# Kernel optimization log

Measured on AMD Instinct MI355X. Metric: run time of the kernel, lower is better.

The kernel has to match this reference:

```python
import jax, jax.numpy as jnp
import numpy as np

N = 100000   # num nodes
E = 3200000  # num edges (avg degree 32)
EPS = 1e-5   # BatchNorm eps


def _gcn_norm(edge_index, edge_weight, n):
    # add self loops with weight 1 (PyG gcn_norm default fill_value=1.0)
    loops = jnp.arange(n, dtype=edge_index.dtype)
    ei = jnp.concatenate([edge_index, jnp.stack([loops, loops])], axis=1)
    ew = jnp.concatenate([edge_weight, jnp.ones((n,), edge_weight.dtype)])
    row, col = ei[0], ei[1]
    deg = jax.ops.segment_sum(ew, col, num_segments=n)
    deg_safe = jnp.where(deg > 0, deg, 1.0)
    dinv = jnp.where(deg > 0, jax.lax.rsqrt(deg_safe), 0.0)
    norm = dinv[row] * ew * dinv[col]  # [E+N]
    return row, col, norm


def _gcn_conv(x, row, col, norm, W, b, n):
    h = x @ W                                   # [N, out]
    msg = h[row] * norm[:, None]                # gather + scale, [E+N, out]
    out = jax.ops.segment_sum(msg, col, num_segments=n)  # scatter-add
    return out + b


def _bn(x, g, b, rm, rv):
    # BatchNorm1d in eval mode: running statistics
    return (x - rm) * jax.lax.rsqrt(rv + EPS) * g + b


def setup_inputs() -> dict:
    key = jax.random.key(0)
    ks = jax.random.split(key, 24)
    def p(i, shape, scale=1.0):
        return jax.random.normal(ks[i], shape, dtype=jnp.float32) * scale
    inp = {
        "x": p(0, (N, 1)),
        "edge_index": jax.random.randint(ks[1], (2, E), 0, N, dtype=jnp.int32),
        "edge_weight": jax.random.uniform(ks[2], (E,), dtype=jnp.float32),
        # GCNConv weights (glorot-ish scale) and biases
        "W1": p(3, (1, 16), 0.5), "b1": jnp.zeros((16,), jnp.float32),
        "W2": p(4, (16, 4), 0.25), "b2": jnp.zeros((4,), jnp.float32),
        "W3": p(5, (4, 1), 0.5), "b3": jnp.zeros((1,), jnp.float32),
        # BatchNorm params + running stats (running_var > 0)
        "g1": p(6, (16,), 0.1) + 1.0, "be1": p(7, (16,), 0.1),
        "rm1": p(8, (16,), 0.1), "rv1": jax.random.uniform(ks[9], (16,)) + 0.5,
        "g2": p(10, (4,), 0.1) + 1.0, "be2": p(11, (4,), 0.1),
        "rm2": p(12, (4,), 0.1), "rv2": jax.random.uniform(ks[13], (4,)) + 0.5,
        "g3": p(14, (1,), 0.1) + 1.0, "be3": p(15, (1,), 0.1),
        "rm3": p(16, (1,), 0.1), "rv3": jax.random.uniform(ks[17], (1,)) + 0.5,
        # end Linear(1, 1)
        "Wl": p(18, (1, 1)), "bl": p(19, (1,), 0.1),
    }
    return inp


def reference(x, edge_index, edge_weight,
              W1, b1, W2, b2, W3, b3,
              g1, be1, rm1, rv1,
              g2, be2, rm2, rv2,
              g3, be3, rm3, rv3,
              Wl, bl):
    row, col, norm = _gcn_norm(edge_index, edge_weight, N)
    h = _gcn_conv(x, row, col, norm, W1, b1, N)
    h = jax.nn.relu(_bn(h, g1, be1, rm1, rv1))  # dropout = identity in eval
    h = _gcn_conv(h, row, col, norm, W2, b2, N)
    h = jax.nn.relu(_bn(h, g2, be2, rm2, rv2))
    h = _gcn_conv(h, row, col, norm, W3, b3, N)
    h = _bn(h, g3, be3, rm3, rv3)
    h = h @ Wl + bl
    return jax.nn.sigmoid(h)
```

## Files before the change

### kernel.cpp

```cpp
#include <hip/hip_runtime.h>
#include <math.h>

#define NN 100000
#define NE 3200000
#define EPSBN 1e-5f

#define BSH 7
#define NB 782
#define NBLK 500
#define CHUNK 6400
#define C4 (CHUNK/4)
#define CAP 5120
#define BTA 512

#define NSB 12512
#define STCAP 4608

__global__ void k_params_zero(const float* __restrict__ W1, const float* __restrict__ b1,
                              const float* __restrict__ g1, const float* __restrict__ be1,
                              const float* __restrict__ rm1, const float* __restrict__ rv1,
                              const float* __restrict__ b2,
                              const float* __restrict__ g2, const float* __restrict__ be2,
                              const float* __restrict__ rm2, const float* __restrict__ rv2,
                              const float* __restrict__ b3,
                              const float* __restrict__ g3, const float* __restrict__ be3,
                              const float* __restrict__ rm3, const float* __restrict__ rv3,
                              const float* __restrict__ Wl, const float* __restrict__ bl,
                              float* __restrict__ P, int* __restrict__ cnt) {
    int f = threadIdx.x;
    for (int i = f; i < NB; i += 1024) cnt[i] = 0;
    if (f < 16) {
        float k = g1[f] * rsqrtf(rv1[f] + EPSBN);
        P[f]      = W1[f] * k;
        P[16 + f] = (b1[f] - rm1[f]) * k + be1[f];
    }
    if (f < 4) {
        float k = g2[f] * rsqrtf(rv2[f] + EPSBN);
        P[32 + f] = k;
        P[36 + f] = (b2[f] - rm2[f]) * k + be2[f];
    }
    if (f == 0) {
        float k = g3[0] * rsqrtf(rv3[0] + EPSBN);
        P[40] = k * Wl[0];
        P[41] = ((b3[0] - rm3[0]) * k + be3[0]) * Wl[0] + bl[0];
    }
}

__global__ void k_build(const int* __restrict__ row, const int* __restrict__ col,
                        const float* __restrict__ ew, int* __restrict__ cnt,
                        uint2* __restrict__ rec) {
    __shared__ int h[NB];
    __shared__ int gb[NB];
    __shared__ int gsum[98];
    __shared__ uint2 st[CHUNK];
    __shared__ unsigned short sb[CHUNK];
    int blk = blockIdx.x, tid = threadIdx.x;
    for (int j = tid; j < NB; j += BTA) h[j] = 0;
    __syncthreads();

    const int4* c4 = (const int4*)(col + blk * CHUNK);
    int rk[4][4];
#pragma unroll
    for (int it = 0; it < 4; ++it) {
        int i = tid + it * BTA;
        if (i < C4) {
            int4 c = c4[i];
            rk[it][0] = atomicAdd(&h[c.x >> BSH], 1);
            rk[it][1] = atomicAdd(&h[c.y >> BSH], 1);
            rk[it][2] = atomicAdd(&h[c.z >> BSH], 1);
            rk[it][3] = atomicAdd(&h[c.w >> BSH], 1);
        }
    }
    __syncthreads();

    for (int j = tid; j < NB; j += BTA) {
        int hj = h[j];
        gb[j] = hj ? atomicAdd(&cnt[j], hj) : 0;
    }

    if (tid < 98) {
        int s = 0, b0 = tid * 8;
#pragma unroll
        for (int k = 0; k < 8; ++k) { int idx = b0 + k; s += (idx < NB) ? h[idx] : 0; }
        gsum[tid] = s;
    }
    __syncthreads();
    if (tid == 0) {
        int run = 0;
        for (int g = 0; g < 98; ++g) { int t = gsum[g]; gsum[g] = run; run += t; }
    }
    __syncthreads();
    if (tid < 98) {
        int run = gsum[tid], b0 = tid * 8;
#pragma unroll
        for (int k = 0; k < 8; ++k) {
            int idx = b0 + k;
            if (idx < NB) { int t = h[idx]; h[idx] = run; run += t; }
        }
    }
    __syncthreads();

    const int4*   r4 = (const int4*)(row + blk * CHUNK);
    const float4* w4 = (const float4*)(ew + blk * CHUNK);
#pragma unroll
    for (int it = 0; it < 4; ++it) {
        int i = tid + it * BTA;
        if (i < C4) {
            int4 c = c4[i]; int4 r = r4[i]; float4 w = w4[i];
            int b0 = c.x >> BSH, b1 = c.y >> BSH, b2 = c.z >> BSH, b3 = c.w >> BSH;
            int s0 = h[b0] + rk[it][0];
            st[s0] = make_uint2((unsigned)r.x | ((unsigned)(c.x & 127) << 17), __float_as_uint(w.x));
            sb[s0] = (unsigned short)b0;
            int s1 = h[b1] + rk[it][1];
            st[s1] = make_uint2((unsigned)r.y | ((unsigned)(c.y & 127) << 17), __float_as_uint(w.y));
            sb[s1] = (unsigned short)b1;
            int s2 = h[b2] + rk[it][2];
            st[s2] = make_uint2((unsigned)r.z | ((unsigned)(c.z & 127) << 17), __float_as_uint(w.z));
            sb[s2] = (unsigned short)b2;
            int s3 = h[b3] + rk[it][3];
            st[s3] = make_uint2((unsigned)r.w | ((unsigned)(c.w & 127) << 17), __float_as_uint(w.w));
            sb[s3] = (unsigned short)b3;
        }
    }
    __syncthreads();

    for (int i = tid; i < CHUNK; i += BTA) {
        int b = sb[i];
        rec[(size_t)b * CAP + gb[b] + (i - h[b])] = st[i];
    }
}

__global__ void k_subsort_deg(const int* __restrict__ cnt, uint2* __restrict__ rec,
                              int2* __restrict__ subsn, const float* __restrict__ x,
                              float* __restrict__ dinv, float* __restrict__ xd) {
    __shared__ uint2 st[STCAP];
    __shared__ int subtot[16];
    __shared__ int live[16];
    __shared__ int sstart[16];
    __shared__ int scount[16];
    int bin = blockIdx.x, tid = threadIdx.x;
    int lane = tid & 63, wv = tid >> 6;
    int n = cnt[bin];
    if (n > STCAP) n = STCAP;
    uint2* rb = rec + (size_t)bin * CAP;
    for (int i = tid; i < n; i += BTA) st[i] = rb[i];
    if (tid < 16) subtot[tid] = 0;
    __syncthreads();

    int myCnt = 0;
    for (int base = tid - lane; base < n; base += BTA) {
        int i = base + lane;
        bool v = (i < n);
        unsigned key = v ? ((st[i].x >> 20) & 15u) : 0u;
        unsigned long long bv = __ballot(v);
        unsigned long long b0 = __ballot(key & 1u);
        unsigned long long b1 = __ballot(key & 2u);
        unsigned long long b2 = __ballot(key & 4u);
        unsigned long long b3 = __ballot(key & 8u);
        if (lane < 16) {
            unsigned k = (unsigned)lane;
            unsigned long long m = bv;
            m &= (k & 1u) ? b0 : ~b0;
            m &= (k & 2u) ? b1 : ~b1;
            m &= (k & 4u) ? b2 : ~b2;
            m &= (k & 8u) ? b3 : ~b3;
            myCnt += __popcll(m);
        }
    }
    if (lane < 16 && myCnt) atomicAdd(&subtot[lane], myCnt);
    __syncthreads();

    if (tid == 0) {
        int run = 0;
        for (int k = 0; k < 16; ++k) {
            live[k] = run;
            sstart[k] = run;
            scount[k] = subtot[k];
            subsn[bin * 16 + k] = make_int2(bin * CAP + run, subtot[k]);
            run += subtot[k];
        }
    }
    __syncthreads();

    for (int base = tid - lane; base < n; base += BTA) {
        int i = base + lane;
        bool v = (i < n);
        uint2 rcd = v ? st[i] : make_uint2(0u, 0u);
        unsigned key = v ? ((rcd.x >> 20) & 15u) : 0u;
        unsigned long long bv = __ballot(v);
        unsigned long long b0 = __ballot(key & 1u);
        unsigned long long b1 = __ballot(key & 2u);
        unsigned long long b2 = __ballot(key & 4u);
        unsigned long long b3 = __ballot(key & 8u);
        int gb = 0;
        if (lane < 16) {
            unsigned k = (unsigned)lane;
            unsigned long long m = bv;
            m &= (k & 1u) ? b0 : ~b0;
            m &= (k & 2u) ? b1 : ~b1;
            m &= (k & 4u) ? b2 : ~b2;
            m &= (k & 8u) ? b3 : ~b3;
            int c = __popcll(m);
            if (c) gb = atomicAdd(&live[(int)k], c);
        }
        unsigned long long same = bv;
        same &= (key & 1u) ? b0 : ~b0;
        same &= (key & 2u) ? b1 : ~b1;
        same &= (key & 4u) ? b2 : ~b2;
        same &= (key & 8u) ? b3 : ~b3;
        unsigned long long below = (lane == 0) ? 0ull : ((~0ull) >> (64 - lane));
        int rank = __popcll(same & below);
        int mybase = __shfl(gb, (int)key);
        if (v) rb[mybase + rank] = rcd;
    }
    __syncthreads();

    for (int s = 0; s < 2; ++s) {
        int sb = (wv << 1) | s;
        int n0 = scount[sb];
        const uint2* p = rb + sstart[sb];
        float acc[8] = {0.f, 0.f, 0.f, 0.f, 0.f, 0.f, 0.f, 0.f};
        for (int i = lane; i < n0; i += 64) {
            uint2 v = p[i];
            int cl = (v.x >> 17) & 7;
            float w = __uint_as_float(v.y);
#pragma unroll
            for (int c = 0; c < 8; ++c) acc[c] += (cl == c) ? w : 0.f;
        }
#pragma unroll
        for (int c = 0; c < 8; ++c) {
            float a = acc[c];
            a += __shfl_xor(a, 1);  a += __shfl_xor(a, 2);  a += __shfl_xor(a, 4);
            a += __shfl_xor(a, 8);  a += __shfl_xor(a, 16); a += __shfl_xor(a, 32);
            acc[c] = a;
        }
        float mine = acc[0];
#pragma unroll
        for (int c = 1; c < 8; ++c) mine = (lane == c) ? acc[c] : mine;
        int colv = (bin << BSH) + (sb << 3) + lane;
        if (lane < 8 && colv < NN) {
            float d = rsqrtf(1.0f + mine);
            dinv[colv] = d;
            xd[colv] = x[colv] * d;
        }
    }
}


__global__ void k_agg1_2(const int2* __restrict__ subsn, const uint2* __restrict__ rec,
                         const float* __restrict__ dinv, const float* __restrict__ xd,
                         const float* __restrict__ P, const float* __restrict__ W2,
                         float* __restrict__ m2s) {
    __shared__ float sacc[8][8][32];
    int tid = threadIdx.x, lane = tid & 63, wv = tid >> 6;
    int b = blockIdx.x * 8 + wv;
    int2 sn = subsn[b];
    float acc[8] = {0.f, 0.f, 0.f, 0.f, 0.f, 0.f, 0.f, 0.f};
    for (int i = lane; i < sn.y; i += 64) {
        uint2 v = rec[sn.x + i];
        int cl = (v.x >> 17) & 7;
        float g = xd[v.x & 0x1FFFF] * __uint_as_float(v.y);
#pragma unroll
        for (int c = 0; c < 8; ++c) acc[c] += (cl == c) ? g : 0.f;
    }
#pragma unroll
    for (int c = 0; c < 8; ++c) acc[c] += __shfl_xor(acc[c], 32);
    if (lane < 32) {
#pragma unroll
        for (int c = 0; c < 8; ++c) sacc[wv][c][lane] = acc[c];
    }
    __syncthreads();
    if (tid < 64) {
        int w8 = tid >> 3, c = tid & 7;
        float s = 0.f;
        for (int l = 0; l < 32; ++l) s += sacc[w8][c][(l + tid) & 31];
        int colv = blockIdx.x * 64 + tid;
        if (colv < NN) {
            float dc = dinv[colv];
            float y = (s + xd[colv]) * dc;
            float m0 = 0.f, m1 = 0.f, m2v = 0.f, m3v = 0.f;
#pragma unroll
            for (int f = 0; f < 16; ++f) {
                float z = fmaxf(fmaf(y, P[f], P[16 + f]), 0.0f);
                m0 = fmaf(z, W2[f * 4 + 0], m0);
                m1 = fmaf(z, W2[f * 4 + 1], m1);
                m2v = fmaf(z, W2[f * 4 + 2], m2v);
                m3v = fmaf(z, W2[f * 4 + 3], m3v);
            }
            *(float4*)(m2s + 4 * colv) = make_float4(m0 * dc, m1 * dc, m2v * dc, m3v * dc);
        }
    }
}

__global__ void k_agg2_2(const int2* __restrict__ subsn, const uint2* __restrict__ rec,
                         const float* __restrict__ dinv, const float* __restrict__ m2s,
                         const float* __restrict__ P, const float* __restrict__ W3,
                         float* __restrict__ m3s) {
    __shared__ float sacc[8][8][4][32];
    __shared__ float sfin[8][8][4];
    int tid = threadIdx.x, lane = tid & 63, wv = tid >> 6;
    int b = blockIdx.x * 8 + wv;
    int2 sn = subsn[b];
    float acc[8][4];
#pragma unroll
    for (int c = 0; c < 8; ++c)
#pragma unroll
        for (int j = 0; j < 4; ++j) acc[c][j] = 0.f;
    for (int i = lane; i < sn.y; i += 64) {
        uint2 v = rec[sn.x + i];
        int cl = (v.x >> 17) & 7;
        float w = __uint_as_float(v.y);
        float4 m = *(const float4*)(m2s + 4 * (v.x & 0x1FFFF));
#pragma unroll
        for (int c = 0; c < 8; ++c) {
            float sel = (cl == c) ? w : 0.f;
            acc[c][0] = fmaf(m.x, sel, acc[c][0]);
            acc[c][1] = fmaf(m.y, sel, acc[c][1]);
            acc[c][2] = fmaf(m.z, sel, acc[c][2]);
            acc[c][3] = fmaf(m.w, sel, acc[c][3]);
        }
    }
#pragma unroll
    for (int c = 0; c < 8; ++c)
#pragma unroll
        for (int j = 0; j < 4; ++j) acc[c][j] += __shfl_xor(acc[c][j], 32);
    if (lane < 32) {
#pragma unroll
        for (int c = 0; c < 8; ++c)
#pragma unroll
            for (int j = 0; j < 4; ++j) sacc[wv][c][j][lane] = acc[c][j];
    }
    __syncthreads();
    if (tid < 256) {
        int w8 = tid >> 5, c = (tid >> 2) & 7, j = tid & 3;
        float s = 0.f;
        for (int l = 0; l < 32; ++l) s += sacc[w8][c][j][(l + tid) & 31];
        sfin[w8][c][j] = s;
    }
    __syncthreads();
    if (tid < 64) {
        int w8 = tid >> 3, c = tid & 7;
        int colv = blockIdx.x * 64 + tid;
        if (colv < NN) {
            float dc = dinv[colv];
            float4 mc = *(const float4*)(m2s + 4 * colv);
            float a0 = (sfin[w8][c][0] + mc.x) * dc;
            float a1 = (sfin[w8][c][1] + mc.y) * dc;
            float a2 = (sfin[w8][c][2] + mc.z) * dc;
            float a3 = (sfin[w8][c][3] + mc.w) * dc;
            float v3 = 0.f;
            v3 = fmaf(fmaxf(fmaf(a0, P[32], P[36]), 0.f), W3[0], v3);
            v3 = fmaf(fmaxf(fmaf(a1, P[33], P[37]), 0.f), W3[1], v3);
            v3 = fmaf(fmaxf(fmaf(a2, P[34], P[38]), 0.f), W3[2], v3);
            v3 = fmaf(fmaxf(fmaf(a3, P[35], P[39]), 0.f), W3[3], v3);
            m3s[colv] = v3 * dc;
        }
    }
}

__global__ void k_agg3_2(const int2* __restrict__ subsn, const uint2* __restrict__ rec,
                         const float* __restrict__ dinv, const float* __restrict__ m3s,
                         const float* __restrict__ P, float* __restrict__ out) {
    __shared__ float sacc[8][8][32];
    int tid = threadIdx.x, lane = tid & 63, wv = tid >> 6;
    int b = blockIdx.x * 8 + wv;
    int2 sn = subsn[b];
    float acc[8] = {0.f, 0.f, 0.f, 0.f, 0.f, 0.f, 0.f, 0.f};
    for (int i = lane; i < sn.y; i += 64) {
        uint2 v = rec[sn.x + i];
        int cl = (v.x >> 17) & 7;
        float g = m3s[v.x & 0x1FFFF] * __uint_as_float(v.y);
#pragma unroll
        for (int c = 0; c < 8; ++c) acc[c] += (cl == c) ? g : 0.f;
    }
#pragma unroll
    for (int c = 0; c < 8; ++c) acc[c] += __shfl_xor(acc[c], 32);
    if (lane < 32) {
#pragma unroll
        for (int c = 0; c < 8; ++c) sacc[wv][c][lane] = acc[c];
    }
    __syncthreads();
    if (tid < 64) {
        int w8 = tid >> 3, c = tid & 7;
        float s = 0.f;
        for (int l = 0; l < 32; ++l) s += sacc[w8][c][(l + tid) & 31];
        int colv = blockIdx.x * 64 + tid;
        if (colv < NN) {
            float t = fmaf((s + m3s[colv]) * dinv[colv], P[40], P[41]);
            out[colv] = 1.0f / (1.0f + __expf(-t));
        }
    }
}


__global__ void k_init_deg(float* __restrict__ deg) {
    int i = blockIdx.x * blockDim.x + threadIdx.x;
    if (i < NN) deg[i] = 1.0f;
}

__global__ void k_dinv_y1(const float* __restrict__ deg, const float* __restrict__ x,
                          float* __restrict__ dinv, float* __restrict__ y1) {
    int i = blockIdx.x * blockDim.x + threadIdx.x;
    if (i >= NN) return;
    float d = rsqrtf(deg[i]);
    dinv[i] = d;
    y1[i] = x[i] * d * d;
}

__global__ void k_l1_epi(const float* __restrict__ y1, const float* __restrict__ dinv,
                         const float* __restrict__ P, const float* __restrict__ W2,
                         float* __restrict__ m2, float* __restrict__ agg2) {
    int i = blockIdx.x * blockDim.x + threadIdx.x;
    if (i >= NN) return;
    float y = y1[i];
    float m0 = 0.f, m1 = 0.f, m2v = 0.f, m3v = 0.f;
#pragma unroll
    for (int f = 0; f < 16; ++f) {
        float z = fmaxf(fmaf(y, P[f], P[16 + f]), 0.0f);
        m0 = fmaf(z, W2[f * 4 + 0], m0);
        m1 = fmaf(z, W2[f * 4 + 1], m1);
        m2v = fmaf(z, W2[f * 4 + 2], m2v);
        m3v = fmaf(z, W2[f * 4 + 3], m3v);
    }
    float d = dinv[i];
    float d2 = d * d;
    *(float4*)(m2 + 4 * i)   = make_float4(m0, m1, m2v, m3v);
    *(float4*)(agg2 + 4 * i) = make_float4(m0 * d2, m1 * d2, m2v * d2, m3v * d2);
}

__global__ void k_l2_epi(const float* __restrict__ agg2, const float* __restrict__ dinv,
                         const float* __restrict__ P, const float* __restrict__ W3,
                         float* __restrict__ m3, float* __restrict__ agg3) {
    int i = blockIdx.x * blockDim.x + threadIdx.x;
    if (i >= NN) return;
    float4 a = *(const float4*)(agg2 + 4 * i);
    float v = 0.f;
    v = fmaf(fmaxf(fmaf(a.x, P[32], P[36]), 0.f), W3[0], v);
    v = fmaf(fmaxf(fmaf(a.y, P[33], P[37]), 0.f), W3[1], v);
    v = fmaf(fmaxf(fmaf(a.z, P[34], P[38]), 0.f), W3[2], v);
    v = fmaf(fmaxf(fmaf(a.w, P[35], P[39]), 0.f), W3[3], v);
    float d = dinv[i];
    m3[i] = v;
    agg3[i] = v * d * d;
}

__global__ void k_final(const float* __restrict__ agg3, const float* __restrict__ P,
                        float* __restrict__ out) {
    int i = blockIdx.x * blockDim.x + threadIdx.x;
    if (i >= NN) return;
    float t = fmaf(agg3[i], P[40], P[41]);
    out[i] = 1.0f / (1.0f + __expf(-t));
}

__global__ void k_deg(const int* __restrict__ col, const float* __restrict__ ew,
                      float* __restrict__ deg) {
    int e = (blockIdx.x * blockDim.x + threadIdx.x) * 4;
    if (e >= NE) return;
    int4 c = *(const int4*)(col + e);
    float4 w = *(const float4*)(ew + e);
    atomicAdd(&deg[c.x], w.x);
    atomicAdd(&deg[c.y], w.y);
    atomicAdd(&deg[c.z], w.z);
    atomicAdd(&deg[c.w], w.w);
}

__global__ void k_norm_agg1(const int* __restrict__ row, const int* __restrict__ col,
                            const float* __restrict__ ew, const float* __restrict__ dinv,
                            const float* __restrict__ x,
                            float* __restrict__ norm, float* __restrict__ y1) {
    int e = (blockIdx.x * blockDim.x + threadIdx.x) * 4;
    if (e >= NE) return;
    int4 r = *(const int4*)(row + e);
    int4 c = *(const int4*)(col + e);
    float4 w = *(const float4*)(ew + e);
    float4 nv;
    nv.x = dinv[r.x] * w.x * dinv[c.x];
    nv.y = dinv[r.y] * w.y * dinv[c.y];
    nv.z = dinv[r.z] * w.z * dinv[c.z];
    nv.w = dinv[r.w] * w.w * dinv[c.w];
    *(float4*)(norm + e) = nv;
    atomicAdd(&y1[c.x], x[r.x] * nv.x);
    atomicAdd(&y1[c.y], x[r.y] * nv.y);
    atomicAdd(&y1[c.z], x[r.z] * nv.z);
    atomicAdd(&y1[c.w], x[r.w] * nv.w);
}

__global__ void k_agg2(const int* __restrict__ row, const int* __restrict__ col,
                       const float* __restrict__ norm, const float* __restrict__ m2,
                       float* __restrict__ agg2) {
    int e = blockIdx.x * blockDim.x + threadIdx.x;
    if (e >= NE) return;
    int r = row[e], c = col[e];
    float nv = norm[e];
    float4 m = *(const float4*)(m2 + 4 * r);
    atomicAdd(&agg2[4 * c + 0], m.x * nv);
    atomicAdd(&agg2[4 * c + 1], m.y * nv);
    atomicAdd(&agg2[4 * c + 2], m.z * nv);
    atomicAdd(&agg2[4 * c + 3], m.w * nv);
}

__global__ void k_agg3(const int* __restrict__ row, const int* __restrict__ col,
                       const float* __restrict__ norm, const float* __restrict__ m3,
                       float* __restrict__ agg3) {
    int e = (blockIdx.x * blockDim.x + threadIdx.x) * 4;
    if (e >= NE) return;
    int4 r = *(const int4*)(row + e);
    int4 c = *(const int4*)(col + e);
    float4 nv = *(const float4*)(norm + e);
    atomicAdd(&agg3[c.x], m3[r.x] * nv.x);
    atomicAdd(&agg3[c.y], m3[r.y] * nv.y);
    atomicAdd(&agg3[c.z], m3[r.z] * nv.z);
    atomicAdd(&agg3[c.w], m3[r.w] * nv.w);
}


extern "C" void kernel_launch(void* const* d_in, const int* in_sizes, int n_in,
                              void* d_out, int out_size, void* d_ws, size_t ws_size,
                              hipStream_t stream) {
    const float* x  = (const float*)d_in[0];
    const int*   ei = (const int*)d_in[1];
    const float* ew = (const float*)d_in[2];
    const float* W1 = (const float*)d_in[3];
    const float* b1 = (const float*)d_in[4];
    const float* W2 = (const float*)d_in[5];
    const float* b2 = (const float*)d_in[6];
    const float* W3 = (const float*)d_in[7];
    const float* b3 = (const float*)d_in[8];
    const float* g1 = (const float*)d_in[9];
    const float* be1 = (const float*)d_in[10];
    const float* rm1 = (const float*)d_in[11];
    const float* rv1 = (const float*)d_in[12];
    const float* g2 = (const float*)d_in[13];
    const float* be2 = (const float*)d_in[14];
    const float* rm2 = (const float*)d_in[15];
    const float* rv2 = (const float*)d_in[16];
    const float* g3 = (const float*)d_in[17];
    const float* be3 = (const float*)d_in[18];
    const float* rm3 = (const float*)d_in[19];
    const float* rv3 = (const float*)d_in[20];
    const float* Wl = (const float*)d_in[21];
    const float* bl = (const float*)d_in[22];
    float* out = (float*)d_out;

    const int* row = ei;
    const int* col = ei + NE;

    const int BT = 256;
    const int gN = (NN + BT - 1) / BT;
    const int gE4 = (NE / 4 + BT - 1) / BT;

    char* ws = (char*)d_ws;

    if (ws_size >= 37000000u) {
        float* P     = (float*)(ws);
        int*   cnt   = (int*)  (ws + 4096);
        int2*  subsn = (int2*) (ws + 16384);
        float* dinv  = (float*)(ws + 524288);
        float* xd    = (float*)(ws + 1048576);
        float* m3s   = (float*)(ws + 1572864);
        float* m2s   = (float*)(ws + 2097152);
        uint2* rec   = (uint2*)(ws + 4194304);

        k_params_zero<<<1, 1024, 0, stream>>>(W1, b1, g1, be1, rm1, rv1,
                                              b2, g2, be2, rm2, rv2,
                                              b3, g3, be3, rm3, rv3, Wl, bl, P, cnt);
        k_build<<<NBLK, BTA, 0, stream>>>(row, col, ew, cnt, rec);
        k_subsort_deg<<<NB, BTA, 0, stream>>>(cnt, rec, subsn, x, dinv, xd);
        k_agg1_2<<<NSB / 8, BTA, 0, stream>>>(subsn, rec, dinv, xd, P, W2, m2s);
        k_agg2_2<<<NSB / 8, BTA, 0, stream>>>(subsn, rec, dinv, m2s, P, W3, m3s);
        k_agg3_2<<<NSB / 8, BTA, 0, stream>>>(subsn, rec, dinv, m3s, P, out);
    } else {
        float* deg   = (float*)(ws);
        float* dinv  = (float*)(ws + 400000);
        float* y1    = (float*)(ws + 800000);
        float* m2    = (float*)(ws + 1200000);
        float* agg2  = (float*)(ws + 2800000);
        float* m3    = (float*)(ws + 4400000);
        float* agg3  = (float*)(ws + 4800000);
        float* Pf    = (float*)(ws + 5200000);
        float* norm  = (float*)(ws + 5200256);
        const int gE1 = (NE + BT - 1) / BT;

        k_params_zero<<<1, 1024, 0, stream>>>(W1, b1, g1, be1, rm1, rv1,
                                              b2, g2, be2, rm2, rv2,
                                              b3, g3, be3, rm3, rv3, Wl, bl, Pf, (int*)(ws + 5300000));
        k_init_deg<<<gN, BT, 0, stream>>>(deg);
        k_deg<<<gE4, BT, 0, stream>>>(col, ew, deg);
        k_dinv_y1<<<gN, BT, 0, stream>>>(deg, x, dinv, y1);
        k_norm_agg1<<<gE4, BT, 0, stream>>>(row, col, ew, dinv, x, norm, y1);
        k_l1_epi<<<gN, BT, 0, stream>>>(y1, dinv, Pf, W2, m2, agg2);
        k_agg2<<<(NE + BT - 1) / BT, BT, 0, stream>>>(row, col, norm, m2, agg2);
        k_l2_epi<<<gN, BT, 0, stream>>>(agg2, dinv, Pf, W3, m3, agg3);
        k_agg3<<<gE4, BT, 0, stream>>>(row, col, norm, m3, agg3);
        k_final<<<gN, BT, 0, stream>>>(agg3, Pf, out);
    }
}
```

Measured before the change: 121.7 us.

## Fuse subsort and three aggregation layers into one cooperative persistent kernel

Replaces the subsort and three per-layer aggregation kernels with a single cooperative kernel of 391 blocks. Each block owns two bins and keeps their sorted edge records resident in shared memory across all layers, with grid.sync between the layers. This removes three kernel launches and the repeated global reloads of the edge records, and unrolls the gather loops by two. The fused kernel needs about 74KB of shared memory per block and a co-resident grid; if the cooperative launch fails it falls back to the old kernels. The low-workspace fallback path is deleted.

```diff
diff --git a/kernel.cpp b/kernel.cpp
--- a/kernel.cpp
+++ b/kernel.cpp
@@ -1,5 +1,8 @@
 #include <hip/hip_runtime.h>
+#include <hip/hip_cooperative_groups.h>
 #include <math.h>
+
+namespace cg = cooperative_groups;
 
 #define NN 100000
 #define NE 3200000
@@ -15,6 +18,13 @@
 
 #define NSB 12512
 #define STCAP 4608
+#define FB 391
+
+__device__ __forceinline__ float wave_allreduce(float a) {
+    a += __shfl_xor(a, 1);  a += __shfl_xor(a, 2);  a += __shfl_xor(a, 4);
+    a += __shfl_xor(a, 8);  a += __shfl_xor(a, 16); a += __shfl_xor(a, 32);
+    return a;
+}
 
 __global__ void k_params_zero(const float* __restrict__ W1, const float* __restrict__ b1,
                               const float* __restrict__ g1, const float* __restrict__ be1,
@@ -130,6 +140,298 @@
     }
 }
 
+__global__ void __launch_bounds__(512, 4)
+k_fused(const int* __restrict__ cnt, const uint2* __restrict__ rec,
+        const float* __restrict__ x, float* __restrict__ dinv, float* __restrict__ xd,
+        float* __restrict__ m2s, float* __restrict__ m3s,
+        const float* __restrict__ P, const float* __restrict__ W2,
+        const float* __restrict__ W3, float* __restrict__ out) {
+    __shared__ uint2 st[2][STCAP];
+    __shared__ int subtot[2][16];
+    __shared__ int live[2][16];
+    __shared__ int sstart[2][16];
+    __shared__ int scount[2][16];
+
+    cg::grid_group grid = cg::this_grid();
+    int tid = threadIdx.x, lane = tid & 63, wv = tid >> 6;
+    int blk = blockIdx.x;
+
+    for (int b2 = 0; b2 < 2; ++b2) {
+        int bin = blk * 2 + b2;
+        int n = cnt[bin]; if (n > STCAP) n = STCAP;
+        const uint2* rb = rec + (size_t)bin * CAP;
+        uint2 r[9];
+#pragma unroll
+        for (int k = 0; k < 9; ++k) {
+            int i = tid + k * BTA;
+            if (i < n) r[k] = rb[i];
+        }
+        if (tid < 16) subtot[b2][tid] = 0;
+        __syncthreads();
+
+        int myCnt = 0;
+#pragma unroll
+        for (int k = 0; k < 9; ++k) {
+            int i = tid + k * BTA;
+            bool v = (i < n);
+            unsigned key = v ? ((r[k].x >> 20) & 15u) : 0u;
+            unsigned long long bv = __ballot(v);
+            unsigned long long q0 = __ballot(key & 1u);
+            unsigned long long q1 = __ballot(key & 2u);
+            unsigned long long q2 = __ballot(key & 4u);
+            unsigned long long q3 = __ballot(key & 8u);
+            if (lane < 16) {
+                unsigned kk = (unsigned)lane;
+                unsigned long long m = bv;
+                m &= (kk & 1u) ? q0 : ~q0;
+                m &= (kk & 2u) ? q1 : ~q1;
+                m &= (kk & 4u) ? q2 : ~q2;
+                m &= (kk & 8u) ? q3 : ~q3;
+                myCnt += __popcll(m);
+            }
+        }
+        if (lane < 16 && myCnt) atomicAdd(&subtot[b2][lane], myCnt);
+        __syncthreads();
+
+        if (tid == 0) {
+            int run = 0;
+            for (int k2 = 0; k2 < 16; ++k2) {
+                live[b2][k2] = run;
+                sstart[b2][k2] = run;
+                scount[b2][k2] = subtot[b2][k2];
+                run += subtot[b2][k2];
+            }
+        }
+        __syncthreads();
+
+#pragma unroll
+        for (int k = 0; k < 9; ++k) {
+            int i = tid + k * BTA;
+            bool v = (i < n);
+            uint2 rcd = v ? r[k] : make_uint2(0u, 0u);
+            unsigned key = v ? ((rcd.x >> 20) & 15u) : 0u;
+            unsigned long long bv = __ballot(v);
+            unsigned long long q0 = __ballot(key & 1u);
+            unsigned long long q1 = __ballot(key & 2u);
+            unsigned long long q2 = __ballot(key & 4u);
+            unsigned long long q3 = __ballot(key & 8u);
+            int gb = 0;
+            if (lane < 16) {
+                unsigned kk = (unsigned)lane;
+                unsigned long long m = bv;
+                m &= (kk & 1u) ? q0 : ~q0;
+                m &= (kk & 2u) ? q1 : ~q1;
+                m &= (kk & 4u) ? q2 : ~q2;
+                m &= (kk & 8u) ? q3 : ~q3;
+                int c = __popcll(m);
+                if (c) gb = atomicAdd(&live[b2][(int)kk], c);
+            }
+            unsigned long long same = bv;
+            same &= (key & 1u) ? q0 : ~q0;
+            same &= (key & 2u) ? q1 : ~q1;
+            same &= (key & 4u) ? q2 : ~q2;
+            same &= (key & 8u) ? q3 : ~q3;
+            unsigned long long below = (lane == 0) ? 0ull : ((~0ull) >> (64 - lane));
+            int rank = __popcll(same & below);
+            int mybase = __shfl(gb, (int)key);
+            if (v) st[b2][mybase + rank] = rcd;
+        }
+        __syncthreads();
+    }
+
+    for (int b2 = 0; b2 < 2; ++b2) {
+        int bin = blk * 2 + b2;
+        for (int s = 0; s < 2; ++s) {
+            int sbx = (wv << 1) | s;
+            int n0 = scount[b2][sbx];
+            const uint2* p = &st[b2][sstart[b2][sbx]];
+            float acc[8] = {0.f, 0.f, 0.f, 0.f, 0.f, 0.f, 0.f, 0.f};
+            for (int i = lane; i < n0; i += 64) {
+                uint2 v = p[i];
+                int cl = (v.x >> 17) & 7;
+                float w = __uint_as_float(v.y);
+#pragma unroll
+                for (int c = 0; c < 8; ++c) acc[c] += (cl == c) ? w : 0.f;
+            }
+#pragma unroll
+            for (int c = 0; c < 8; ++c) acc[c] = wave_allreduce(acc[c]);
+            float mine = acc[0];
+#pragma unroll
+            for (int c = 1; c < 8; ++c) mine = (lane == c) ? acc[c] : mine;
+            int colv = (bin << BSH) + (sbx << 3) + lane;
+            if (lane < 8 && colv < NN) {
+                float d = rsqrtf(1.0f + mine);
+                dinv[colv] = d;
+                xd[colv] = x[colv] * d;
+            }
+        }
+    }
+    grid.sync();
+
+    for (int b2 = 0; b2 < 2; ++b2) {
+        int bin = blk * 2 + b2;
+        for (int s = 0; s < 2; ++s) {
+            int sbx = (wv << 1) | s;
+            int n0 = scount[b2][sbx];
+            const uint2* p = &st[b2][sstart[b2][sbx]];
+            float acc[8] = {0.f, 0.f, 0.f, 0.f, 0.f, 0.f, 0.f, 0.f};
+            int i = lane;
+            for (; i + 64 < n0; i += 128) {
+                uint2 v0 = p[i], v1 = p[i + 64];
+                float g0 = xd[v0.x & 0x1FFFF] * __uint_as_float(v0.y);
+                float g1 = xd[v1.x & 0x1FFFF] * __uint_as_float(v1.y);
+                int c0 = (v0.x >> 17) & 7, c1 = (v1.x >> 17) & 7;
+#pragma unroll
+                for (int c = 0; c < 8; ++c) {
+                    acc[c] += (c0 == c) ? g0 : 0.f;
+                    acc[c] += (c1 == c) ? g1 : 0.f;
+                }
+            }
+            for (; i < n0; i += 64) {
+                uint2 v = p[i];
+                float g = xd[v.x & 0x1FFFF] * __uint_as_float(v.y);
+                int cl = (v.x >> 17) & 7;
+#pragma unroll
+                for (int c = 0; c < 8; ++c) acc[c] += (cl == c) ? g : 0.f;
+            }
+#pragma unroll
+            for (int c = 0; c < 8; ++c) acc[c] = wave_allreduce(acc[c]);
+            float mine = acc[0];
+#pragma unroll
+            for (int c = 1; c < 8; ++c) mine = (lane == c) ? acc[c] : mine;
+            int colv = (bin << BSH) + (sbx << 3) + lane;
+            if (lane < 8 && colv < NN) {
+                float dc = dinv[colv];
+                float y = (mine + xd[colv]) * dc;
+                float m0 = 0.f, m1 = 0.f, m2v = 0.f, m3v = 0.f;
+#pragma unroll
+                for (int f = 0; f < 16; ++f) {
+                    float z = fmaxf(fmaf(y, P[f], P[16 + f]), 0.0f);
+                    m0 = fmaf(z, W2[f * 4 + 0], m0);
+                    m1 = fmaf(z, W2[f * 4 + 1], m1);
+                    m2v = fmaf(z, W2[f * 4 + 2], m2v);
+                    m3v = fmaf(z, W2[f * 4 + 3], m3v);
+                }
+                *(float4*)(m2s + 4 * colv) = make_float4(m0 * dc, m1 * dc, m2v * dc, m3v * dc);
+            }
+        }
+    }
+    grid.sync();
+
+    for (int b2 = 0; b2 < 2; ++b2) {
+        int bin = blk * 2 + b2;
+        for (int s = 0; s < 2; ++s) {
+            int sbx = (wv << 1) | s;
+            int n0 = scount[b2][sbx];
+            const uint2* p = &st[b2][sstart[b2][sbx]];
+            float acc[8][4];
+#pragma unroll
+            for (int c = 0; c < 8; ++c)
+#pragma unroll
+                for (int j = 0; j < 4; ++j) acc[c][j] = 0.f;
+            int i = lane;
+            for (; i + 64 < n0; i += 128) {
+                uint2 v0 = p[i], v1 = p[i + 64];
+                float w0 = __uint_as_float(v0.y), w1 = __uint_as_float(v1.y);
+                float4 ma = *(const float4*)(m2s + 4 * (v0.x & 0x1FFFF));
+                float4 mb = *(const float4*)(m2s + 4 * (v1.x & 0x1FFFF));
+                int c0 = (v0.x >> 17) & 7, c1 = (v1.x >> 17) & 7;
+#pragma unroll
+                for (int c = 0; c < 8; ++c) {
+                    float s0 = (c0 == c) ? w0 : 0.f;
+                    float s1 = (c1 == c) ? w1 : 0.f;
+                    acc[c][0] = fmaf(ma.x, s0, fmaf(mb.x, s1, acc[c][0]));
+                    acc[c][1] = fmaf(ma.y, s0, fmaf(mb.y, s1, acc[c][1]));
+                    acc[c][2] = fmaf(ma.z, s0, fmaf(mb.z, s1, acc[c][2]));
+                    acc[c][3] = fmaf(ma.w, s0, fmaf(mb.w, s1, acc[c][3]));
+                }
+            }
+            for (; i < n0; i += 64) {
+                uint2 v = p[i];
+                float w = __uint_as_float(v.y);
+                float4 m = *(const float4*)(m2s + 4 * (v.x & 0x1FFFF));
+                int cl = (v.x >> 17) & 7;
+#pragma unroll
+                for (int c = 0; c < 8; ++c) {
+                    float sel = (cl == c) ? w : 0.f;
+                    acc[c][0] = fmaf(m.x, sel, acc[c][0]);
+                    acc[c][1] = fmaf(m.y, sel, acc[c][1]);
+                    acc[c][2] = fmaf(m.z, sel, acc[c][2]);
+                    acc[c][3] = fmaf(m.w, sel, acc[c][3]);
+                }
+            }
+#pragma unroll
+            for (int c = 0; c < 8; ++c)
+#pragma unroll
+                for (int j = 0; j < 4; ++j) acc[c][j] = wave_allreduce(acc[c][j]);
+            float r0 = acc[0][0], r1 = acc[0][1], r2 = acc[0][2], r3 = acc[0][3];
+#pragma unroll
+            for (int c = 1; c < 8; ++c) {
+                r0 = (lane == c) ? acc[c][0] : r0;
+                r1 = (lane == c) ? acc[c][1] : r1;
+                r2 = (lane == c) ? acc[c][2] : r2;
+                r3 = (lane == c) ? acc[c][3] : r3;
+            }
+            int colv = (bin << BSH) + (sbx << 3) + lane;
+            if (lane < 8 && colv < NN) {
+                float dc = dinv[colv];
+                float4 mc = *(const float4*)(m2s + 4 * colv);
+                float a0 = (r0 + mc.x) * dc;
+                float a1 = (r1 + mc.y) * dc;
+                float a2 = (r2 + mc.z) * dc;
+                float a3 = (r3 + mc.w) * dc;
+                float v3 = 0.f;
+                v3 = fmaf(fmaxf(fmaf(a0, P[32], P[36]), 0.f), W3[0], v3);
+                v3 = fmaf(fmaxf(fmaf(a1, P[33], P[37]), 0.f), W3[1], v3);
+                v3 = fmaf(fmaxf(fmaf(a2, P[34], P[38]), 0.f), W3[2], v3);
+                v3 = fmaf(fmaxf(fmaf(a3, P[35], P[39]), 0.f), W3[3], v3);
+                m3s[colv] = v3 * dc;
+            }
+        }
+    }
+    grid.sync();
+
+    for (int b2 = 0; b2 < 2; ++b2) {
+        int bin = blk * 2 + b2;
+        for (int s = 0; s < 2; ++s) {
+            int sbx = (wv << 1) | s;
+            int n0 = scount[b2][sbx];
+            const uint2* p = &st[b2][sstart[b2][sbx]];
+            float acc[8] = {0.f, 0.f, 0.f, 0.f, 0.f, 0.f, 0.f, 0.f};
+            int i = lane;
+            for (; i + 64 < n0; i += 128) {
+                uint2 v0 = p[i], v1 = p[i + 64];
+                float g0 = m3s[v0.x & 0x1FFFF] * __uint_as_float(v0.y);
+                float g1 = m3s[v1.x & 0x1FFFF] * __uint_as_float(v1.y);
+                int c0 = (v0.x >> 17) & 7, c1 = (v1.x >> 17) & 7;
+#pragma unroll
+                for (int c = 0; c < 8; ++c) {
+                    acc[c] += (c0 == c) ? g0 : 0.f;
+                    acc[c] += (c1 == c) ? g1 : 0.f;
+                }
+            }
+            for (; i < n0; i += 64) {
+                uint2 v = p[i];
+                float g = m3s[v.x & 0x1FFFF] * __uint_as_float(v.y);
+                int cl = (v.x >> 17) & 7;
+#pragma unroll
+                for (int c = 0; c < 8; ++c) acc[c] += (cl == c) ? g : 0.f;
+            }
+#pragma unroll
+            for (int c = 0; c < 8; ++c) acc[c] = wave_allreduce(acc[c]);
+            float mine = acc[0];
+#pragma unroll
+            for (int c = 1; c < 8; ++c) mine = (lane == c) ? acc[c] : mine;
+            int colv = (bin << BSH) + (sbx << 3) + lane;
+            if (lane < 8 && colv < NN) {
+                float t = fmaf((mine + m3s[colv]) * dinv[colv], P[40], P[41]);
+                out[colv] = 1.0f / (1.0f + __expf(-t));
+            }
+        }
+    }
+}
+
+
 __global__ void k_subsort_deg(const int* __restrict__ cnt, uint2* __restrict__ rec,
                               int2* __restrict__ subsn, const float* __restrict__ x,
                               float* __restrict__ dinv, float* __restrict__ xd) {
@@ -153,17 +455,17 @@
         bool v = (i < n);
         unsigned key = v ? ((st[i].x >> 20) & 15u) : 0u;
         unsigned long long bv = __ballot(v);
-        unsigned long long b0 = __ballot(key & 1u);
-        unsigned long long b1 = __ballot(key & 2u);
-        unsigned long long b2 = __ballot(key & 4u);
-        unsigned long long b3 = __ballot(key & 8u);
+        unsigned long long q0 = __ballot(key & 1u);
+        unsigned long long q1 = __ballot(key & 2u);
+        unsigned long long q2 = __ballot(key & 4u);
+        unsigned long long q3 = __ballot(key & 8u);
         if (lane < 16) {
             unsigned k = (unsigned)lane;
             unsigned long long m = bv;
-            m &= (k & 1u) ? b0 : ~b0;
-            m &= (k & 2u) ? b1 : ~b1;
-            m &= (k & 4u) ? b2 : ~b2;
-            m &= (k & 8u) ? b3 : ~b3;
+            m &= (k & 1u) ? q0 : ~q0;
+            m &= (k & 2u) ? q1 : ~q1;
+            m &= (k & 4u) ? q2 : ~q2;
+            m &= (k & 8u) ? q3 : ~q3;
             myCnt += __popcll(m);
         }
     }
@@ -173,9 +475,7 @@
     if (tid == 0) {
         int run = 0;
         for (int k = 0; k < 16; ++k) {
-            live[k] = run;
-            sstart[k] = run;
-            scount[k] = subtot[k];
+            live[k] = run; sstart[k] = run; scount[k] = subtot[k];
             subsn[bin * 16 + k] = make_int2(bin * CAP + run, subtot[k]);
             run += subtot[k];
         }
@@ -188,26 +488,26 @@
         uint2 rcd = v ? st[i] : make_uint2(0u, 0u);
         unsigned key = v ? ((rcd.x >> 20) & 15u) : 0u;
         unsigned long long bv = __ballot(v);
-        unsigned long long b0 = __ballot(key & 1u);
-        unsigned long long b1 = __ballot(key & 2u);
-        unsigned long long b2 = __ballot(key & 4u);
-        unsigned long long b3 = __ballot(key & 8u);
+        unsigned long long q0 = __ballot(key & 1u);
+        unsigned long long q1 = __ballot(key & 2u);
+        unsigned long long q2 = __ballot(key & 4u);
+        unsigned long long q3 = __ballot(key & 8u);
         int gb = 0;
         if (lane < 16) {
             unsigned k = (unsigned)lane;
             unsigned long long m = bv;
-            m &= (k & 1u) ? b0 : ~b0;
-            m &= (k & 2u) ? b1 : ~b1;
-            m &= (k & 4u) ? b2 : ~b2;
-            m &= (k & 8u) ? b3 : ~b3;
+            m &= (k & 1u) ? q0 : ~q0;
+            m &= (k & 2u) ? q1 : ~q1;
+            m &= (k & 4u) ? q2 : ~q2;
+            m &= (k & 8u) ? q3 : ~q3;
             int c = __popcll(m);
             if (c) gb = atomicAdd(&live[(int)k], c);
         }
         unsigned long long same = bv;
-        same &= (key & 1u) ? b0 : ~b0;
-        same &= (key & 2u) ? b1 : ~b1;
-        same &= (key & 4u) ? b2 : ~b2;
-        same &= (key & 8u) ? b3 : ~b3;
+        same &= (key & 1u) ? q0 : ~q0;
+        same &= (key & 2u) ? q1 : ~q1;
+        same &= (key & 4u) ? q2 : ~q2;
+        same &= (key & 8u) ? q3 : ~q3;
         unsigned long long below = (lane == 0) ? 0ull : ((~0ull) >> (64 - lane));
         int rank = __popcll(same & below);
         int mybase = __shfl(gb, (int)key);
@@ -216,9 +516,9 @@
     __syncthreads();
 
     for (int s = 0; s < 2; ++s) {
-        int sb = (wv << 1) | s;
-        int n0 = scount[sb];
-        const uint2* p = rb + sstart[sb];
+        int sbx = (wv << 1) | s;
+        int n0 = scount[sbx];
+        const uint2* p = rb + sstart[sbx];
         float acc[8] = {0.f, 0.f, 0.f, 0.f, 0.f, 0.f, 0.f, 0.f};
         for (int i = lane; i < n0; i += 64) {
             uint2 v = p[i];
@@ -228,16 +528,11 @@
             for (int c = 0; c < 8; ++c) acc[c] += (cl == c) ? w : 0.f;
         }
 #pragma unroll
-        for (int c = 0; c < 8; ++c) {
-            float a = acc[c];
-            a += __shfl_xor(a, 1);  a += __shfl_xor(a, 2);  a += __shfl_xor(a, 4);
-            a += __shfl_xor(a, 8);  a += __shfl_xor(a, 16); a += __shfl_xor(a, 32);
-            acc[c] = a;
-        }
+        for (int c = 0; c < 8; ++c) acc[c] = wave_allreduce(acc[c]);
         float mine = acc[0];
 #pragma unroll
         for (int c = 1; c < 8; ++c) mine = (lane == c) ? acc[c] : mine;
-        int colv = (bin << BSH) + (sb << 3) + lane;
+        int colv = (bin << BSH) + (sbx << 3) + lane;
         if (lane < 8 && colv < NN) {
             float d = rsqrtf(1.0f + mine);
             dinv[colv] = d;
@@ -246,49 +541,41 @@
     }
 }
 
-
 __global__ void k_agg1_2(const int2* __restrict__ subsn, const uint2* __restrict__ rec,
                          const float* __restrict__ dinv, const float* __restrict__ xd,
                          const float* __restrict__ P, const float* __restrict__ W2,
                          float* __restrict__ m2s) {
-    __shared__ float sacc[8][8][32];
     int tid = threadIdx.x, lane = tid & 63, wv = tid >> 6;
     int b = blockIdx.x * 8 + wv;
     int2 sn = subsn[b];
     float acc[8] = {0.f, 0.f, 0.f, 0.f, 0.f, 0.f, 0.f, 0.f};
+    const uint2* p = rec + sn.x;
     for (int i = lane; i < sn.y; i += 64) {
-        uint2 v = rec[sn.x + i];
+        uint2 v = p[i];
         int cl = (v.x >> 17) & 7;
         float g = xd[v.x & 0x1FFFF] * __uint_as_float(v.y);
 #pragma unroll
         for (int c = 0; c < 8; ++c) acc[c] += (cl == c) ? g : 0.f;
     }
 #pragma unroll
-    for (int c = 0; c < 8; ++c) acc[c] += __shfl_xor(acc[c], 32);
-    if (lane < 32) {
-#pragma unroll
-        for (int c = 0; c < 8; ++c) sacc[wv][c][lane] = acc[c];
-    }
-    __syncthreads();
-    if (tid < 64) {
-        int w8 = tid >> 3, c = tid & 7;
-        float s = 0.f;
-        for (int l = 0; l < 32; ++l) s += sacc[w8][c][(l + tid) & 31];
-        int colv = blockIdx.x * 64 + tid;
-        if (colv < NN) {
-            float dc = dinv[colv];
-            float y = (s + xd[colv]) * dc;
-            float m0 = 0.f, m1 = 0.f, m2v = 0.f, m3v = 0.f;
-#pragma unroll
-            for (int f = 0; f < 16; ++f) {
-                float z = fmaxf(fmaf(y, P[f], P[16 + f]), 0.0f);
-                m0 = fmaf(z, W2[f * 4 + 0], m0);
-                m1 = fmaf(z, W2[f * 4 + 1], m1);
-                m2v = fmaf(z, W2[f * 4 + 2], m2v);
-                m3v = fmaf(z, W2[f * 4 + 3], m3v);
-            }
-            *(float4*)(m2s + 4 * colv) = make_float4(m0 * dc, m1 * dc, m2v * dc, m3v * dc);
-        }
+    for (int c = 0; c < 8; ++c) acc[c] = wave_allreduce(acc[c]);
+    float mine = acc[0];
+#pragma unroll
+    for (int c = 1; c < 8; ++c) mine = (lane == c) ? acc[c] : mine;
+    int colv = b * 8 + lane;
+    if (lane < 8 && colv < NN) {
+        float dc = dinv[colv];
+        float y = (mine + xd[colv]) * dc;
+        float m0 = 0.f, m1 = 0.f, m2v = 0.f, m3v = 0.f;
+#pragma unroll
+        for (int f = 0; f < 16; ++f) {
+            float z = fmaxf(fmaf(y, P[f], P[16 + f]), 0.0f);
+            m0 = fmaf(z, W2[f * 4 + 0], m0);
+            m1 = fmaf(z, W2[f * 4 + 1], m1);
+            m2v = fmaf(z, W2[f * 4 + 2], m2v);
+            m3v = fmaf(z, W2[f * 4 + 3], m3v);
+        }
+        *(float4*)(m2s + 4 * colv) = make_float4(m0 * dc, m1 * dc, m2v * dc, m3v * dc);
     }
 }
 
@@ -296,8 +583,6 @@
                          const float* __restrict__ dinv, const float* __restrict__ m2s,
                          const float* __restrict__ P, const float* __restrict__ W3,
                          float* __restrict__ m3s) {
-    __shared__ float sacc[8][8][4][32];
-    __shared__ float sfin[8][8][4];
     int tid = threadIdx.x, lane = tid & 63, wv = tid >> 6;
     int b = blockIdx.x * 8 + wv;
     int2 sn = subsn[b];
@@ -306,8 +591,9 @@
     for (int c = 0; c < 8; ++c)
 #pragma unroll
         for (int j = 0; j < 4; ++j) acc[c][j] = 0.f;
+    const uint2* p = rec + sn.x;
     for (int i = lane; i < sn.y; i += 64) {
-        uint2 v = rec[sn.x + i];
+        uint2 v = p[i];
         int cl = (v.x >> 17) & 7;
         float w = __uint_as_float(v.y);
         float4 m = *(const float4*)(m2s + 4 * (v.x & 0x1FFFF));
@@ -323,194 +609,57 @@
 #pragma unroll
     for (int c = 0; c < 8; ++c)
 #pragma unroll
-        for (int j = 0; j < 4; ++j) acc[c][j] += __shfl_xor(acc[c][j], 32);
-    if (lane < 32) {
-#pragma unroll
-        for (int c = 0; c < 8; ++c)
-#pragma unroll
-            for (int j = 0; j < 4; ++j) sacc[wv][c][j][lane] = acc[c][j];
-    }
-    __syncthreads();
-    if (tid < 256) {
-        int w8 = tid >> 5, c = (tid >> 2) & 7, j = tid & 3;
-        float s = 0.f;
-        for (int l = 0; l < 32; ++l) s += sacc[w8][c][j][(l + tid) & 31];
-        sfin[w8][c][j] = s;
-    }
-    __syncthreads();
-    if (tid < 64) {
-        int w8 = tid >> 3, c = tid & 7;
-        int colv = blockIdx.x * 64 + tid;
-        if (colv < NN) {
-            float dc = dinv[colv];
-            float4 mc = *(const float4*)(m2s + 4 * colv);
-            float a0 = (sfin[w8][c][0] + mc.x) * dc;
-            float a1 = (sfin[w8][c][1] + mc.y) * dc;
-            float a2 = (sfin[w8][c][2] + mc.z) * dc;
-            float a3 = (sfin[w8][c][3] + mc.w) * dc;
-            float v3 = 0.f;
-            v3 = fmaf(fmaxf(fmaf(a0, P[32], P[36]), 0.f), W3[0], v3);
-            v3 = fmaf(fmaxf(fmaf(a1, P[33], P[37]), 0.f), W3[1], v3);
-            v3 = fmaf(fmaxf(fmaf(a2, P[34], P[38]), 0.f), W3[2], v3);
-            v3 = fmaf(fmaxf(fmaf(a3, P[35], P[39]), 0.f), W3[3], v3);
-            m3s[colv] = v3 * dc;
-        }
+        for (int j = 0; j < 4; ++j) acc[c][j] = wave_allreduce(acc[c][j]);
+    float r0 = acc[0][0], r1 = acc[0][1], r2 = acc[0][2], r3 = acc[0][3];
+#pragma unroll
+    for (int c = 1; c < 8; ++c) {
+        r0 = (lane == c) ? acc[c][0] : r0;
+        r1 = (lane == c) ? acc[c][1] : r1;
+        r2 = (lane == c) ? acc[c][2] : r2;
+        r3 = (lane == c) ? acc[c][3] : r3;
+    }
+    int colv = b * 8 + lane;
+    if (lane < 8 && colv < NN) {
+        float dc = dinv[colv];
+        float4 mc = *(const float4*)(m2s + 4 * colv);
+        float a0 = (r0 + mc.x) * dc;
+        float a1 = (r1 + mc.y) * dc;
+        float a2 = (r2 + mc.z) * dc;
+        float a3 = (r3 + mc.w) * dc;
+        float v3 = 0.f;
+        v3 = fmaf(fmaxf(fmaf(a0, P[32], P[36]), 0.f), W3[0], v3);
+        v3 = fmaf(fmaxf(fmaf(a1, P[33], P[37]), 0.f), W3[1], v3);
+        v3 = fmaf(fmaxf(fmaf(a2, P[34], P[38]), 0.f), W3[2], v3);
+        v3 = fmaf(fmaxf(fmaf(a3, P[35], P[39]), 0.f), W3[3], v3);
+        m3s[colv] = v3 * dc;
     }
 }
 
 __global__ void k_agg3_2(const int2* __restrict__ subsn, const uint2* __restrict__ rec,
                          const float* __restrict__ dinv, const float* __restrict__ m3s,
                          const float* __restrict__ P, float* __restrict__ out) {
-    __shared__ float sacc[8][8][32];
     int tid = threadIdx.x, lane = tid & 63, wv = tid >> 6;
     int b = blockIdx.x * 8 + wv;
     int2 sn = subsn[b];
     float acc[8] = {0.f, 0.f, 0.f, 0.f, 0.f, 0.f, 0.f, 0.f};
+    const uint2* p = rec + sn.x;
     for (int i = lane; i < sn.y; i += 64) {
-        uint2 v = rec[sn.x + i];
+        uint2 v = p[i];
         int cl = (v.x >> 17) & 7;
         float g = m3s[v.x & 0x1FFFF] * __uint_as_float(v.y);
 #pragma unroll
         for (int c = 0; c < 8; ++c) acc[c] += (cl == c) ? g : 0.f;
     }
 #pragma unroll
-    for (int c = 0; c < 8; ++c) acc[c] += __shfl_xor(acc[c], 32);
-    if (lane < 32) {
-#pragma unroll
-        for (int c = 0; c < 8; ++c) sacc[wv][c][lane] = acc[c];
-    }
-    __syncthreads();
-    if (tid < 64) {
-        int w8 = tid >> 3, c = tid & 7;
-        float s = 0.f;
-        for (int l = 0; l < 32; ++l) s += sacc[w8][c][(l + tid) & 31];
-        int colv = blockIdx.x * 64 + tid;
-        if (colv < NN) {
-            float t = fmaf((s + m3s[colv]) * dinv[colv], P[40], P[41]);
-            out[colv] = 1.0f / (1.0f + __expf(-t));
-        }
-    }
-}
-
-
-__global__ void k_init_deg(float* __restrict__ deg) {
-    int i = blockIdx.x * blockDim.x + threadIdx.x;
-    if (i < NN) deg[i] = 1.0f;
-}
-
-__global__ void k_dinv_y1(const float* __restrict__ deg, const float* __restrict__ x,
-                          float* __restrict__ dinv, float* __restrict__ y1) {
-    int i = blockIdx.x * blockDim.x + threadIdx.x;
-    if (i >= NN) return;
-    float d = rsqrtf(deg[i]);
-    dinv[i] = d;
-    y1[i] = x[i] * d * d;
-}
-
-__global__ void k_l1_epi(const float* __restrict__ y1, const float* __restrict__ dinv,
-                         const float* __restrict__ P, const float* __restrict__ W2,
-                         float* __restrict__ m2, float* __restrict__ agg2) {
-    int i = blockIdx.x * blockDim.x + threadIdx.x;
-    if (i >= NN) return;
-    float y = y1[i];
-    float m0 = 0.f, m1 = 0.f, m2v = 0.f, m3v = 0.f;
-#pragma unroll
-    for (int f = 0; f < 16; ++f) {
-        float z = fmaxf(fmaf(y, P[f], P[16 + f]), 0.0f);
-        m0 = fmaf(z, W2[f * 4 + 0], m0);
-        m1 = fmaf(z, W2[f * 4 + 1], m1);
-        m2v = fmaf(z, W2[f * 4 + 2], m2v);
-        m3v = fmaf(z, W2[f * 4 + 3], m3v);
-    }
-    float d = dinv[i];
-    float d2 = d * d;
-    *(float4*)(m2 + 4 * i)   = make_float4(m0, m1, m2v, m3v);
-    *(float4*)(agg2 + 4 * i) = make_float4(m0 * d2, m1 * d2, m2v * d2, m3v * d2);
-}
-
-__global__ void k_l2_epi(const float* __restrict__ agg2, const float* __restrict__ dinv,
-                         const float* __restrict__ P, const float* __restrict__ W3,
-                         float* __restrict__ m3, float* __restrict__ agg3) {
-    int i = blockIdx.x * blockDim.x + threadIdx.x;
-    if (i >= NN) return;
-    float4 a = *(const float4*)(agg2 + 4 * i);
-    float v = 0.f;
-    v = fmaf(fmaxf(fmaf(a.x, P[32], P[36]), 0.f), W3[0], v);
-    v = fmaf(fmaxf(fmaf(a.y, P[33], P[37]), 0.f), W3[1], v);
-    v = fmaf(fmaxf(fmaf(a.z, P[34], P[38]), 0.f), W3[2], v);
-    v = fmaf(fmaxf(fmaf(a.w, P[35], P[39]), 0.f), W3[3], v);
-    float d = dinv[i];
-    m3[i] = v;
-    agg3[i] = v * d * d;
-}
-
-__global__ void k_final(const float* __restrict__ agg3, const float* __restrict__ P,
-                        float* __restrict__ out) {
-    int i = blockIdx.x * blockDim.x + threadIdx.x;
-    if (i >= NN) return;
-    float t = fmaf(agg3[i], P[40], P[41]);
-    out[i] = 1.0f / (1.0f + __expf(-t));
-}
-
-__global__ void k_deg(const int* __restrict__ col, const float* __restrict__ ew,
-                      float* __restrict__ deg) {
-    int e = (blockIdx.x * blockDim.x + threadIdx.x) * 4;
-    if (e >= NE) return;
-    int4 c = *(const int4*)(col + e);
-    float4 w = *(const float4*)(ew + e);
-    atomicAdd(&deg[c.x], w.x);
-    atomicAdd(&deg[c.y], w.y);
-    atomicAdd(&deg[c.z], w.z);
-    atomicAdd(&deg[c.w], w.w);
-}
-
-__global__ void k_norm_agg1(const int* __restrict__ row, const int* __restrict__ col,
-                            const float* __restrict__ ew, const float* __restrict__ dinv,
-                            const float* __restrict__ x,
-                            float* __restrict__ norm, float* __restrict__ y1) {
-    int e = (blockIdx.x * blockDim.x + threadIdx.x) * 4;
-    if (e >= NE) return;
-    int4 r = *(const int4*)(row + e);
-    int4 c = *(const int4*)(col + e);
-    float4 w = *(const float4*)(ew + e);
-    float4 nv;
-    nv.x = dinv[r.x] * w.x * dinv[c.x];
-    nv.y = dinv[r.y] * w.y * dinv[c.y];
-    nv.z = dinv[r.z] * w.z * dinv[c.z];
-    nv.w = dinv[r.w] * w.w * dinv[c.w];
-    *(float4*)(norm + e) = nv;
-    atomicAdd(&y1[c.x], x[r.x] * nv.x);
-    atomicAdd(&y1[c.y], x[r.y] * nv.y);
-    atomicAdd(&y1[c.z], x[r.z] * nv.z);
-    atomicAdd(&y1[c.w], x[r.w] * nv.w);
-}
-
-__global__ void k_agg2(const int* __restrict__ row, const int* __restrict__ col,
-                       const float* __restrict__ norm, const float* __restrict__ m2,
-                       float* __restrict__ agg2) {
-    int e = blockIdx.x * blockDim.x + threadIdx.x;
-    if (e >= NE) return;
-    int r = row[e], c = col[e];
-    float nv = norm[e];
-    float4 m = *(const float4*)(m2 + 4 * r);
-    atomicAdd(&agg2[4 * c + 0], m.x * nv);
-    atomicAdd(&agg2[4 * c + 1], m.y * nv);
-    atomicAdd(&agg2[4 * c + 2], m.z * nv);
-    atomicAdd(&agg2[4 * c + 3], m.w * nv);
-}
-
-__global__ void k_agg3(const int* __restrict__ row, const int* __restrict__ col,
-                       const float* __restrict__ norm, const float* __restrict__ m3,
-                       float* __restrict__ agg3) {
-    int e = (blockIdx.x * blockDim.x + threadIdx.x) * 4;
-    if (e >= NE) return;
-    int4 r = *(const int4*)(row + e);
-    int4 c = *(const int4*)(col + e);
-    float4 nv = *(const float4*)(norm + e);
-    atomicAdd(&agg3[c.x], m3[r.x] * nv.x);
-    atomicAdd(&agg3[c.y], m3[r.y] * nv.y);
-    atomicAdd(&agg3[c.z], m3[r.z] * nv.z);
-    atomicAdd(&agg3[c.w], m3[r.w] * nv.w);
+    for (int c = 0; c < 8; ++c) acc[c] = wave_allreduce(acc[c]);
+    float mine = acc[0];
+#pragma unroll
+    for (int c = 1; c < 8; ++c) mine = (lane == c) ? acc[c] : mine;
+    int colv = b * 8 + lane;
+    if (lane < 8 && colv < NN) {
+        float t = fmaf((mine + m3s[colv]) * dinv[colv], P[40], P[41]);
+        out[colv] = 1.0f / (1.0f + __expf(-t));
+    }
 }
 
 
@@ -545,53 +694,34 @@
     const int* row = ei;
     const int* col = ei + NE;
 
-    const int BT = 256;
-    const int gN = (NN + BT - 1) / BT;
-    const int gE4 = (NE / 4 + BT - 1) / BT;
-
     char* ws = (char*)d_ws;
 
-    if (ws_size >= 37000000u) {
-        float* P     = (float*)(ws);
-        int*   cnt   = (int*)  (ws + 4096);
-        int2*  subsn = (int2*) (ws + 16384);
-        float* dinv  = (float*)(ws + 524288);
-        float* xd    = (float*)(ws + 1048576);
-        float* m3s   = (float*)(ws + 1572864);
-        float* m2s   = (float*)(ws + 2097152);
-        uint2* rec   = (uint2*)(ws + 4194304);
-
-        k_params_zero<<<1, 1024, 0, stream>>>(W1, b1, g1, be1, rm1, rv1,
-                                              b2, g2, be2, rm2, rv2,
-                                              b3, g3, be3, rm3, rv3, Wl, bl, P, cnt);
-        k_build<<<NBLK, BTA, 0, stream>>>(row, col, ew, cnt, rec);
+    float* P     = (float*)(ws);
+    int*   cnt   = (int*)  (ws + 4096);
+    int2*  subsn = (int2*) (ws + 16384);
+    float* dinv  = (float*)(ws + 524288);
+    float* xd    = (float*)(ws + 1048576);
+    float* m3s   = (float*)(ws + 1572864);
+    float* m2s   = (float*)(ws + 2097152);
+    uint2* rec   = (uint2*)(ws + 4194304);
+
+    k_params_zero<<<1, 1024, 0, stream>>>(W1, b1, g1, be1, rm1, rv1,
+                                          b2, g2, be2, rm2, rv2,
+                                          b3, g3, be3, rm3, rv3, Wl, bl, P, cnt);
+    k_build<<<NBLK, BTA, 0, stream>>>(row, col, ew, cnt, rec);
+
+    const int* cnt_c = cnt;
+    const uint2* rec_c = rec;
+    const float* P_c = P;
+    void* kargs[] = { (void*)&cnt_c, (void*)&rec_c, (void*)&x, (void*)&dinv, (void*)&xd,
+                      (void*)&m2s, (void*)&m3s, (void*)&P_c, (void*)&W2, (void*)&W3,
+                      (void*)&out };
+    hipError_t e = hipLaunchCooperativeKernel((void*)k_fused, dim3(FB), dim3(BTA),
+                                              kargs, 0, stream);
+    if (e != hipSuccess) {
         k_subsort_deg<<<NB, BTA, 0, stream>>>(cnt, rec, subsn, x, dinv, xd);
         k_agg1_2<<<NSB / 8, BTA, 0, stream>>>(subsn, rec, dinv, xd, P, W2, m2s);
         k_agg2_2<<<NSB / 8, BTA, 0, stream>>>(subsn, rec, dinv, m2s, P, W3, m3s);
         k_agg3_2<<<NSB / 8, BTA, 0, stream>>>(subsn, rec, dinv, m3s, P, out);
-    } else {
-        float* deg   = (float*)(ws);
-        float* dinv  = (float*)(ws + 400000);
-        float* y1    = (float*)(ws + 800000);
-        float* m2    = (float*)(ws + 1200000);
-        float* agg2  = (float*)(ws + 2800000);
-        float* m3    = (float*)(ws + 4400000);
-        float* agg3  = (float*)(ws + 4800000);
-        float* Pf    = (float*)(ws + 5200000);
-        float* norm  = (float*)(ws + 5200256);
-        const int gE1 = (NE + BT - 1) / BT;
-
-        k_params_zero<<<1, 1024, 0, stream>>>(W1, b1, g1, be1, rm1, rv1,
-                                              b2, g2, be2, rm2, rv2,
-                                              b3, g3, be3, rm3, rv3, Wl, bl, Pf, (int*)(ws + 5300000));
-        k_init_deg<<<gN, BT, 0, stream>>>(deg);
-        k_deg<<<gE4, BT, 0, stream>>>(col, ew, deg);
-        k_dinv_y1<<<gN, BT, 0, stream>>>(deg, x, dinv, y1);
-        k_norm_agg1<<<gE4, BT, 0, stream>>>(row, col, ew, dinv, x, norm, y1);
-        k_l1_epi<<<gN, BT, 0, stream>>>(y1, dinv, Pf, W2, m2, agg2);
-        k_agg2<<<(NE + BT - 1) / BT, BT, 0, stream>>>(row, col, norm, m2, agg2);
-        k_l2_epi<<<gN, BT, 0, stream>>>(agg2, dinv, Pf, W3, m3, agg3);
-        k_agg3<<<gE4, BT, 0, stream>>>(row, col, norm, m3, agg3);
-        k_final<<<gN, BT, 0, stream>>>(agg3, Pf, out);
-    }
-}
+    }
+}
```

Result: slower. 250.7 us (+106.0%).
